# Kernel optimization log

Measured on AMD Instinct MI355X. Metric: run time of the kernel, lower is better.

Reference implementation:

```python
import jax, jax.numpy as jnp
import numpy as np

N = 50000      # nodes
E = 800000     # edges (avg degree 16)
D_IN, D_H, D_OUT = 128, 96, 32


def _lin(x, W, b):
    return x @ W.T + b


def _transformer_conv(x, src, dst, Wq, bq, Wk, bk, Wv, bv, Ws, bs, n):
    # PyG TransformerConv, heads=1: q_i . k_j / sqrt(d), segment softmax over
    # incoming edges of each target node, weighted sum of values, plus skip.
    q = _lin(x, Wq, bq)            # [N, d]
    k = _lin(x, Wk, bk)            # [N, d]
    v = _lin(x, Wv, bv)            # [N, d]
    d = q.shape[-1]
    score = jnp.sum(q[dst] * k[src], axis=-1) / jnp.sqrt(jnp.float32(d))  # [E]
    m = jax.ops.segment_max(score, dst, num_segments=n)                   # [N]
    m = jnp.where(jnp.isneginf(m), 0.0, m)   # isolated nodes
    e = jnp.exp(score - m[dst])                                           # [E]
    denom = jax.ops.segment_sum(e, dst, num_segments=n)                   # [N]
    alpha = e / jnp.maximum(denom[dst], 1e-16)                            # [E]
    agg = jax.ops.segment_sum(alpha[:, None] * v[src], dst, num_segments=n)
    return agg + _lin(x, Ws, bs)   # root weight (skip connection)


def setup_inputs() -> dict:
    key = jax.random.key(0)
    ks = jax.random.split(key, 32)
    x = jax.random.normal(ks[0], (N, D_IN), dtype=jnp.float32)
    edge_index = jax.random.randint(ks[1], (2, E), 0, N, dtype=jnp.int64)
    dims = [(D_IN, D_H), (D_H, D_H), (D_H, D_OUT)]
    inp = {"x": x, "edge_index": edge_index}
    ki = 2
    for li, (fi, fo) in enumerate(dims, start=1):
        s = 1.0 / np.sqrt(fi)
        for nm in ("Wq", "Wk", "Wv", "Ws"):
            inp[f"{nm}{li}"] = jax.random.normal(ks[ki], (fo, fi), dtype=jnp.float32) * s
            ki += 1
        for nm in ("bq", "bk", "bv", "bs"):
            inp[f"{nm}{li}"] = jnp.zeros((fo,), dtype=jnp.float32)
    return inp


def reference(x, edge_index,
              Wq1, Wk1, Wv1, Ws1, bq1, bk1, bv1, bs1,
              Wq2, Wk2, Wv2, Ws2, bq2, bk2, bv2, bs2,
              Wq3, Wk3, Wv3, Ws3, bq3, bk3, bv3, bs3):
    src, dst = edge_index[0], edge_index[1]
    h = jax.nn.relu(_transformer_conv(x, src, dst, Wq1, bq1, Wk1, bk1, Wv1, bv1, Ws1, bs1, N))
    h = jax.nn.relu(_transformer_conv(h, src, dst, Wq2, bq2, Wk2, bk2, Wv2, bv2, Ws2, bs2, N))
    h = _transformer_conv(h, src, dst, Wq3, bq3, Wk3, bk3, Wv3, bv3, Ws3, bs3, N)
    return jax.nn.log_softmax(h, axis=1)
```

## Files before the change

### kernel.cpp

```cpp
#include <hip/hip_runtime.h>
#include <math.h>

typedef __attribute__((ext_vector_type(8))) __bf16 bf16x8;
typedef __attribute__((ext_vector_type(8))) short short8;
typedef __attribute__((ext_vector_type(4))) float f32x4;
typedef unsigned int uint;
typedef unsigned short ushort;
typedef unsigned char uchar;


__device__ inline bf16x8 ld_bf8(const ushort* p){
  short8 s = *reinterpret_cast<const short8*>(p);
  return __builtin_bit_cast(bf16x8, s);
}

__device__ inline ushort f2bf(float f){
  return __builtin_bit_cast(ushort, (__bf16)f);
}
__device__ inline uint pack2bf(float a, float b){
  return (uint)f2bf(a) | ((uint)f2bf(b) << 16);
}
__device__ inline float bf_lo(uint u){ return __builtin_bit_cast(float, u << 16); }
__device__ inline float bf_hi(uint u){ return __builtin_bit_cast(float, u & 0xFFFF0000u); }

template<int S>
__device__ inline float unp8(uint w){
  return __builtin_amdgcn_cvt_f32_fp8((int)w, S);
}
__device__ inline uint pk8(float a, float b, float c, float d){
  int r = 0;
  r = __builtin_amdgcn_cvt_pk_fp8_f32(a, b, r, false);
  r = __builtin_amdgcn_cvt_pk_fp8_f32(c, d, r, true);
  return (uint)r;
}


__global__ __launch_bounds__(256) void k_bucketA(const int* __restrict__ dst,
                                                 int* __restrict__ gbh, int E){
  __shared__ int cnt[256];
  cnt[threadIdx.x] = 0;
  __syncthreads();
  for (int e = blockIdx.x * blockDim.x + threadIdx.x; e < E; e += gridDim.x * blockDim.x)
    atomicAdd(&cnt[dst[e] >> 8], 1);
  __syncthreads();
  int c = cnt[threadIdx.x];
  if (c > 0) atomicAdd(&gbh[threadIdx.x], c);
}

__global__ __launch_bounds__(256) void k_bscan(const int* __restrict__ gbh,
                                               int* __restrict__ gbase,
                                               int* __restrict__ gcur, int NB, int E){
  __shared__ int wsum[4];
  int t = threadIdx.x;
  int c = (t < NB) ? gbh[t] : 0;
  int lane = t & 63, wv = t >> 6;
  int incl = c;
  #pragma unroll
  for (int o = 1; o < 64; o <<= 1){
    int x = __shfl_up(incl, o);
    if (lane >= o) incl += x;
  }
  if (lane == 63) wsum[wv] = incl;
  __syncthreads();
  int woff = 0;
  for (int w = 0; w < wv; ++w) woff += wsum[w];
  int excl = woff + incl - c;
  if (t < NB){ gbase[t] = excl; gcur[t] = excl; }
  if (t == 0) gbase[NB] = E;
}

#define CS_CHUNK 4096
__global__ __launch_bounds__(256) void k_bucketB(const int* __restrict__ src,
                                                 const int* __restrict__ dst,
                                                 int* __restrict__ gcur,
                                                 uint* __restrict__ epack, int E){
  __shared__ int cnt[256];
  __shared__ int wcur[256];
  const int b0 = blockIdx.x * CS_CHUNK;
  const int b1 = (b0 + CS_CHUNK < E) ? b0 + CS_CHUNK : E;
  cnt[threadIdx.x] = 0;
  __syncthreads();
  for (int e = b0 + threadIdx.x; e < b1; e += 256)
    atomicAdd(&cnt[dst[e] >> 8], 1);
  __syncthreads();
  int c = cnt[threadIdx.x];
  int base = (c > 0) ? atomicAdd(&gcur[threadIdx.x], c) : 0;
  wcur[threadIdx.x] = base;
  __syncthreads();
  for (int e = b0 + threadIdx.x; e < b1; e += 256){
    int d = dst[e];
    int s = src[e];
    int pos = atomicAdd(&wcur[d >> 8], 1);
    epack[pos] = ((uint)d << 16) | (uint)(s & 0xFFFF);
  }
}

__global__ __launch_bounds__(256) void k_bucketC(const uint* __restrict__ epack,
                                                 const int* __restrict__ gbase,
                                                 int* __restrict__ offs,
                                                 ushort* __restrict__ srclist,
                                                 int N, int E){
  __shared__ int cnt[256];
  __shared__ int wcur[256];
  __shared__ int wsum[4];
  const int b = blockIdx.x;
  const int lo = gbase[b], hi = gbase[b + 1];
  cnt[threadIdx.x] = 0;
  __syncthreads();
  for (int i = lo + threadIdx.x; i < hi; i += 256)
    atomicAdd(&cnt[(epack[i] >> 16) & 255], 1);
  __syncthreads();
  int c = cnt[threadIdx.x];
  int lane = threadIdx.x & 63, wv = threadIdx.x >> 6;
  int incl = c;
  #pragma unroll
  for (int o = 1; o < 64; o <<= 1){
    int x = __shfl_up(incl, o);
    if (lane >= o) incl += x;
  }
  if (lane == 63) wsum[wv] = incl;
  __syncthreads();
  int woff = 0;
  for (int w = 0; w < wv; ++w) woff += wsum[w];
  int excl = lo + woff + incl - c;
  int d = (b << 8) + threadIdx.x;
  if (d < N) offs[d] = excl;
  wcur[threadIdx.x] = excl;
  __syncthreads();
  for (int i = lo + threadIdx.x; i < hi; i += 256){
    uint ep = epack[i];
    int pos = atomicAdd(&wcur[(ep >> 16) & 255], 1);
    srclist[pos] = (ushort)(ep & 0xFFFF);
  }
  if (b == 0 && threadIdx.x == 0) offs[N] = E;
}


struct WSet { const float* src[12]; ushort* dst[12]; int n[12]; };

__global__ __launch_bounds__(256) void k_castw(WSet ws){
  int m = blockIdx.y;
  int n = ws.n[m];
  const float* s = ws.src[m];
  ushort* d = ws.dst[m];
  for (int i = blockIdx.x * blockDim.x + threadIdx.x; i < n; i += gridDim.x * blockDim.x)
    d[i] = f2bf(s[i]);
}


template<int KT, int NT, bool F32IN>
__global__ __launch_bounds__(256) void k_projmfma(
    const ushort* __restrict__ hin, const float* __restrict__ hinf, int N,
    const ushort* __restrict__ Wq, const ushort* __restrict__ Wk,
    const ushort* __restrict__ Wv, const ushort* __restrict__ Wsk,
    const float* __restrict__ bq, const float* __restrict__ bk,
    const float* __restrict__ bv, const float* __restrict__ bs,
    ushort* __restrict__ qo, uchar* __restrict__ kv8,
    ushort* __restrict__ so, int kvstB)
{
  constexpr int K  = KT * 32;
  constexpr int FO = NT * 16;
  const int wv   = threadIdx.x >> 6;
  const int lane = threadIdx.x & 63;
  const int r16  = lane & 15;
  const int kg   = lane >> 4;

  const ushort* W = (wv == 0) ? Wq : (wv == 1) ? Wk : (wv == 2) ? Wv : Wsk;
  const float*  b = (wv == 0) ? bq : (wv == 1) ? bk : (wv == 2) ? bv : bs;

  bf16x8 bf[NT][KT];
  #pragma unroll
  for (int nt = 0; nt < NT; ++nt)
    #pragma unroll
    for (int kt = 0; kt < KT; ++kt)
      bf[nt][kt] = ld_bf8(W + (size_t)(nt * 16 + r16) * K + kt * 32 + kg * 8);

  float4 bias[NT];
  #pragma unroll
  for (int nt = 0; nt < NT; ++nt)
    bias[nt] = *reinterpret_cast<const float4*>(b + nt * 16 + kg * 4);

  const int MT = N >> 4;
  for (int mt = blockIdx.x; mt < MT; mt += gridDim.x){
    const int row0 = mt * 16;
    bf16x8 af[KT];
    #pragma unroll
    for (int kt = 0; kt < KT; ++kt){
      if constexpr (F32IN){
        const float* xr = hinf + (size_t)(row0 + r16) * K + kt * 32 + kg * 8;
        float4 a = reinterpret_cast<const float4*>(xr)[0];
        float4 c = reinterpret_cast<const float4*>(xr)[1];
        uint4 u;
        u.x = pack2bf(a.x, a.y); u.y = pack2bf(a.z, a.w);
        u.z = pack2bf(c.x, c.y); u.w = pack2bf(c.z, c.w);
        af[kt] = __builtin_bit_cast(bf16x8, u);
      } else {
        af[kt] = ld_bf8(hin + (size_t)(row0 + r16) * K + kt * 32 + kg * 8);
      }
    }

    f32x4 acc[NT];
    #pragma unroll
    for (int nt = 0; nt < NT; ++nt){
      acc[nt][0] = bias[nt].x; acc[nt][1] = bias[nt].y;
      acc[nt][2] = bias[nt].z; acc[nt][3] = bias[nt].w;
    }
    #pragma unroll
    for (int nt = 0; nt < NT; ++nt)
      #pragma unroll
      for (int kt = 0; kt < KT; ++kt)
        acc[nt] = __builtin_amdgcn_mfma_f32_16x16x32_bf16(bf[nt][kt], af[kt], acc[nt], 0, 0, 0);

    const int row = row0 + r16;
    if (wv == 0 || wv == 3){
      ushort* out = (wv == 0) ? qo : so;
      #pragma unroll
      for (int nt = 0; nt < NT; ++nt){
        uint* p = reinterpret_cast<uint*>(out + (size_t)row * FO + nt * 16 + kg * 4);
        p[0] = pack2bf(acc[nt][0], acc[nt][1]);
        p[1] = pack2bf(acc[nt][2], acc[nt][3]);
      }
    } else {
      const int voff = (wv == 2) ? FO : 0;
      #pragma unroll
      for (int nt = 0; nt < NT; ++nt){
        uint u = pk8(acc[nt][0], acc[nt][1], acc[nt][2], acc[nt][3]);
        *reinterpret_cast<uint*>(kv8 + (size_t)row * kvstB + voff + nt * 16 + kg * 4) = u;
      }
    }
  }
}


template<int FO, int MODE>
__global__ __launch_bounds__(256) void k_attn3(
    const ushort* __restrict__ qb, const uchar* __restrict__ kv,
    const ushort* __restrict__ skipb, const int* __restrict__ offs,
    const ushort* __restrict__ srclist, void* __restrict__ outp,
    int N, float scale)
{
  constexpr int G   = 8;
  constexpr int FPL = FO / G;
  constexpr int KW  = FPL / 4;
  constexpr int KVB = 2 * FO;
  const int lane = threadIdx.x & 63;
  const int sub  = lane & 7;
  const int node = (blockIdx.x * (blockDim.x >> 6) + (threadIdx.x >> 6)) * 8 + (lane >> 3);
  const bool nv  = node < N;
  const int nodec = nv ? node : 0;

  const uint2* qrow = reinterpret_cast<const uint2*>(qb + (size_t)nodec * FO + sub * FPL);
  float qf[FPL];
  #pragma unroll
  for (int w = 0; w < KW; ++w){
    uint2 t = qrow[w];
    qf[4 * w]     = bf_lo(t.x); qf[4 * w + 1] = bf_hi(t.x);
    qf[4 * w + 2] = bf_lo(t.y); qf[4 * w + 3] = bf_hi(t.y);
  }

  float m = -INFINITY, l = 0.f;
  float acc[FPL];
  #pragma unroll
  for (int f = 0; f < FPL; ++f) acc[f] = 0.f;

  const int e0 = nv ? offs[node] : 0;
  const int e1 = nv ? offs[node + 1] : 0;

  uint kA[4][KW], vA[4][KW], kB[4][KW], vB[4][KW];

  auto DOLOAD = [&](int eb, uint (*Kr)[KW], uint (*Vr)[KW]){
    #pragma unroll
    for (int i = 0; i < 4; ++i){
      int ee = eb + i;
      int ec = (ee < e1) ? ee : (e1 - 1);
      int j = srclist[ec];
      const uchar* row = kv + (size_t)j * KVB;
      const uint* rk = reinterpret_cast<const uint*>(row + sub * FPL);
      const uint* rv = reinterpret_cast<const uint*>(row + FO + sub * FPL);
      #pragma unroll
      for (int w = 0; w < KW; ++w){
        Kr[i][w] = rk[w];
        Vr[i][w] = rv[w];
      }
    }
  };

  auto COMPUTE = [&](uint (*Kr)[KW], uint (*Vr)[KW], int ebase){
    float s[4];
    #pragma unroll
    for (int i = 0; i < 4; ++i){
      float t = 0.f;
      #pragma unroll
      for (int w = 0; w < KW; ++w){
        uint kwd = Kr[i][w];
        t = fmaf(qf[4 * w],     unp8<0>(kwd), t);
        t = fmaf(qf[4 * w + 1], unp8<1>(kwd), t);
        t = fmaf(qf[4 * w + 2], unp8<2>(kwd), t);
        t = fmaf(qf[4 * w + 3], unp8<3>(kwd), t);
      }
      s[i] = t;
    }
    #pragma unroll
    for (int o = 1; o < G; o <<= 1){
      s[0] += __shfl_xor(s[0], o);
      s[1] += __shfl_xor(s[1], o);
      s[2] += __shfl_xor(s[2], o);
      s[3] += __shfl_xor(s[3], o);
    }
    s[0] = s[0] * scale;
    s[1] = (ebase + 1 < e1) ? s[1] * scale : -1e30f;
    s[2] = (ebase + 2 < e1) ? s[2] * scale : -1e30f;
    s[3] = (ebase + 3 < e1) ? s[3] * scale : -1e30f;

    float mnew = fmaxf(fmaxf(m, s[0]), fmaxf(fmaxf(s[1], s[2]), s[3]));
    float sfac = __expf(m - mnew);
    float p4[4];
    p4[0] = __expf(s[0] - mnew);
    p4[1] = __expf(s[1] - mnew);
    p4[2] = __expf(s[2] - mnew);
    p4[3] = __expf(s[3] - mnew);
    l = l * sfac + (p4[0] + p4[1]) + (p4[2] + p4[3]);
    #pragma unroll
    for (int f = 0; f < FPL; ++f) acc[f] *= sfac;
    #pragma unroll
    for (int i = 0; i < 4; ++i){
      #pragma unroll
      for (int w = 0; w < KW; ++w){
        uint vwd = Vr[i][w];
        acc[4 * w]     = fmaf(p4[i], unp8<0>(vwd), acc[4 * w]);
        acc[4 * w + 1] = fmaf(p4[i], unp8<1>(vwd), acc[4 * w + 1]);
        acc[4 * w + 2] = fmaf(p4[i], unp8<2>(vwd), acc[4 * w + 2]);
        acc[4 * w + 3] = fmaf(p4[i], unp8<3>(vwd), acc[4 * w + 3]);
      }
    }
    m = mnew;
  };

  if (e0 < e1){
    int e = e0;
    DOLOAD(e, kA, vA);
    for (;;){
      int en = e + 4;
      bool more = en < e1;
      if (more) DOLOAD(en, kB, vB);
      COMPUTE(kA, vA, e);
      e = en;
      if (!more) break;
      en = e + 4;
      more = en < e1;
      if (more) DOLOAD(en, kA, vA);
      COMPUTE(kB, vB, e);
      e = en;
      if (!more) break;
    }
  }

  float inv = 1.f / fmaxf(l, 1e-16f);
  const uint2* srow = reinterpret_cast<const uint2*>(skipb + (size_t)nodec * FO + sub * FPL);
  float val[FPL];
  #pragma unroll
  for (int w = 0; w < KW; ++w){
    uint2 t = srow[w];
    val[4 * w]     = bf_lo(t.x) + acc[4 * w] * inv;
    val[4 * w + 1] = bf_hi(t.x) + acc[4 * w + 1] * inv;
    val[4 * w + 2] = bf_lo(t.y) + acc[4 * w + 2] * inv;
    val[4 * w + 3] = bf_hi(t.y) + acc[4 * w + 3] * inv;
  }

  if (MODE == 0){
    if (nv){
      uint2* orow = reinterpret_cast<uint2*>((ushort*)outp + (size_t)node * FO + sub * FPL);
      #pragma unroll
      for (int w = 0; w < KW; ++w){
        uint2 o;
        o.x = pack2bf(fmaxf(val[4 * w], 0.f),     fmaxf(val[4 * w + 1], 0.f));
        o.y = pack2bf(fmaxf(val[4 * w + 2], 0.f), fmaxf(val[4 * w + 3], 0.f));
        orow[w] = o;
      }
    }
  } else {
    float mx = -INFINITY;
    #pragma unroll
    for (int f = 0; f < FPL; ++f) mx = fmaxf(mx, val[f]);
    #pragma unroll
    for (int o = 1; o < G; o <<= 1) mx = fmaxf(mx, __shfl_xor(mx, o));
    float ssum = 0.f;
    #pragma unroll
    for (int f = 0; f < FPL; ++f) ssum += __expf(val[f] - mx);
    #pragma unroll
    for (int o = 1; o < G; o <<= 1) ssum += __shfl_xor(ssum, o);
    float lg = __logf(ssum);
    if (nv){
      float* orow = (float*)outp + (size_t)node * FO + sub * FPL;
      #pragma unroll
      for (int f = 0; f < FPL; ++f) orow[f] = val[f] - mx - lg;
    }
  }
}


extern "C" void kernel_launch(void* const* d_in, const int* in_sizes, int n_in,
                              void* d_out, int out_size, void* d_ws, size_t ws_size,
                              hipStream_t stream)
{
  const float* x  = (const float*)d_in[0];
  const int*   ei = (const int*)d_in[1];
  const int N = in_sizes[0] / 128;
  const int E = in_sizes[1] / 2;

  const float* W1[4]; const float* b1[4];
  const float* W2[4]; const float* b2[4];
  const float* W3[4]; const float* b3[4];
  for (int i = 0; i < 4; ++i){
    W1[i] = (const float*)d_in[2 + i];   b1[i] = (const float*)d_in[6 + i];
    W2[i] = (const float*)d_in[10 + i];  b2[i] = (const float*)d_in[14 + i];
    W3[i] = (const float*)d_in[18 + i];  b3[i] = (const float*)d_in[22 + i];
  }

  size_t off = 0;
  auto alloc = [&](size_t bytes) -> void* {
    void* p = (char*)d_ws + off;
    off = (off + bytes + 255) & ~(size_t)255;
    return p;
  };
  const int NB = (N + 255) / 256;
  int* offs       = (int*)alloc(((size_t)N + 1) * 4);
  int* gbh        = (int*)alloc(256 * 4);
  int* gbase      = (int*)alloc(260 * 4);
  int* gcur       = (int*)alloc(256 * 4);
  uint* epack     = (uint*)alloc((size_t)E * 4);
  ushort* srclist = (ushort*)alloc((size_t)E * 2);
  ushort* qb  = (ushort*)alloc((size_t)N * 96 * 2);
  uchar*  kvb = (uchar*)alloc((size_t)N * 192);
  ushort* sb  = (ushort*)alloc((size_t)N * 96 * 2);
  ushort* hb  = (ushort*)alloc((size_t)N * 128 * 2);
  ushort* wb  = (ushort*)alloc((size_t)98304 * 2);

  ushort* Wb1[4]; ushort* Wb2[4]; ushort* Wb3[4];
  for (int i = 0; i < 4; ++i){
    Wb1[i] = wb + (size_t)i * 12288;
    Wb2[i] = wb + 49152 + (size_t)i * 9216;
    Wb3[i] = wb + 49152 + 36864 + (size_t)i * 3072;
  }

  WSet wset;
  for (int i = 0; i < 4; ++i){
    wset.src[i]     = W1[i]; wset.dst[i]     = Wb1[i]; wset.n[i]     = 12288;
    wset.src[4 + i] = W2[i]; wset.dst[4 + i] = Wb2[i]; wset.n[4 + i] = 9216;
    wset.src[8 + i] = W3[i]; wset.dst[8 + i] = Wb3[i]; wset.n[8 + i] = 3072;
  }
  k_castw<<<dim3(48, 12), dim3(256), 0, stream>>>(wset);

  const int* esrc = ei;
  const int* edst = ei + E;
  hipMemsetAsync(gbh, 0, 256 * 4, stream);
  k_bucketA<<<dim3(392), dim3(256), 0, stream>>>(edst, gbh, E);
  k_bscan<<<dim3(1), dim3(256), 0, stream>>>(gbh, gbase, gcur, NB, E);
  const int nCB = (E + CS_CHUNK - 1) / CS_CHUNK;
  k_bucketB<<<dim3(nCB), dim3(256), 0, stream>>>(esrc, edst, gcur, epack, E);
  k_bucketC<<<dim3(NB), dim3(256), 0, stream>>>(epack, gbase, offs, srclist, N, E);

  float* outf = (float*)d_out;
  const float sc96 = 1.0f / sqrtf(96.f);
  const float sc32 = 1.0f / sqrtf(32.f);

  const int MT = N / 16;
  const int tpb = (MT + 1023) / 1024;
  const int gridP = (MT + tpb - 1) / tpb;
  const int gridA = (N + 31) / 32;

  k_projmfma<4, 6, true><<<dim3(gridP), dim3(256), 0, stream>>>(nullptr, x, N,
      Wb1[0], Wb1[1], Wb1[2], Wb1[3], b1[0], b1[1], b1[2], b1[3],
      qb, kvb, sb, 192);
  k_attn3<96, 0><<<dim3(gridA), dim3(256), 0, stream>>>(qb, kvb, sb, offs, srclist, hb, N, sc96);

  k_projmfma<3, 6, false><<<dim3(gridP), dim3(256), 0, stream>>>(hb, nullptr, N,
      Wb2[0], Wb2[1], Wb2[2], Wb2[3], b2[0], b2[1], b2[2], b2[3],
      qb, kvb, sb, 192);
  k_attn3<96, 0><<<dim3(gridA), dim3(256), 0, stream>>>(qb, kvb, sb, offs, srclist, hb, N, sc96);

  k_projmfma<3, 2, false><<<dim3(gridP), dim3(256), 0, stream>>>(hb, nullptr, N,
      Wb3[0], Wb3[1], Wb3[2], Wb3[3], b3[0], b3[1], b3[2], b3[3],
      qb, kvb, sb, 64);
  k_attn3<32, 1><<<dim3(gridA), dim3(256), 0, stream>>>(qb, kvb, sb, offs, srclist, outf, N, sc32);
}
```

Measured before the change: 199.5 us.

## Stage projection weights in LDS and split matrices across grid y

The projection kernel now assigns one weight matrix per block (blockIdx.y) and stages that matrix in padded shared memory. Each of the four waves processes its own 16-row tile, instead of four waves sharing a tile with one matrix each. B fragments are read from LDS per MFMA rather than held in registers, which lowers register pressure but adds LDS traffic and a per-block weight load. The grid is fixed at 384x4 blocks. The memset of the bucket histogram is also replaced by a tiny zeroing kernel.

```diff
diff --git a/kernel.cpp b/kernel.cpp
--- a/kernel.cpp
+++ b/kernel.cpp
@@ -34,6 +34,10 @@
   return (uint)r;
 }
 
+
+__global__ void k_zero(int* __restrict__ p, int n){
+  if ((int)threadIdx.x < n) p[threadIdx.x] = 0;
+}
 
 __global__ __launch_bounds__(256) void k_bucketA(const int* __restrict__ dst,
                                                  int* __restrict__ gbh, int E){
@@ -159,29 +163,34 @@
     ushort* __restrict__ so, int kvstB)
 {
   constexpr int K  = KT * 32;
+  constexpr int PS = K + 8;
   constexpr int FO = NT * 16;
+  __shared__ ushort wlds[FO * PS];
+
+  const int mat = blockIdx.y;
+  const ushort* W = (mat == 0) ? Wq : (mat == 1) ? Wk : (mat == 2) ? Wv : Wsk;
+  const float*  b = (mat == 0) ? bq : (mat == 1) ? bk : (mat == 2) ? bv : bs;
+
+  for (int idx = threadIdx.x; idx < FO * (K / 8); idx += 256){
+    int row = idx / (K / 8);
+    int c8  = idx - row * (K / 8);
+    *reinterpret_cast<short8*>(&wlds[row * PS + c8 * 8]) =
+        *reinterpret_cast<const short8*>(W + (size_t)row * K + c8 * 8);
+  }
+  __syncthreads();
+
   const int wv   = threadIdx.x >> 6;
   const int lane = threadIdx.x & 63;
   const int r16  = lane & 15;
   const int kg   = lane >> 4;
 
-  const ushort* W = (wv == 0) ? Wq : (wv == 1) ? Wk : (wv == 2) ? Wv : Wsk;
-  const float*  b = (wv == 0) ? bq : (wv == 1) ? bk : (wv == 2) ? bv : bs;
-
-  bf16x8 bf[NT][KT];
-  #pragma unroll
-  for (int nt = 0; nt < NT; ++nt)
-    #pragma unroll
-    for (int kt = 0; kt < KT; ++kt)
-      bf[nt][kt] = ld_bf8(W + (size_t)(nt * 16 + r16) * K + kt * 32 + kg * 8);
-
   float4 bias[NT];
   #pragma unroll
   for (int nt = 0; nt < NT; ++nt)
     bias[nt] = *reinterpret_cast<const float4*>(b + nt * 16 + kg * 4);
 
   const int MT = N >> 4;
-  for (int mt = blockIdx.x; mt < MT; mt += gridDim.x){
+  for (int mt = blockIdx.x * 4 + wv; mt < MT; mt += gridDim.x * 4){
     const int row0 = mt * 16;
     bf16x8 af[KT];
     #pragma unroll
@@ -208,12 +217,14 @@
     #pragma unroll
     for (int nt = 0; nt < NT; ++nt)
       #pragma unroll
-      for (int kt = 0; kt < KT; ++kt)
-        acc[nt] = __builtin_amdgcn_mfma_f32_16x16x32_bf16(bf[nt][kt], af[kt], acc[nt], 0, 0, 0);
+      for (int kt = 0; kt < KT; ++kt){
+        bf16x8 bfr = ld_bf8(&wlds[(nt * 16 + r16) * PS + kt * 32 + kg * 8]);
+        acc[nt] = __builtin_amdgcn_mfma_f32_16x16x32_bf16(bfr, af[kt], acc[nt], 0, 0, 0);
+      }
 
     const int row = row0 + r16;
-    if (wv == 0 || wv == 3){
-      ushort* out = (wv == 0) ? qo : so;
+    if (mat == 0 || mat == 3){
+      ushort* out = (mat == 0) ? qo : so;
       #pragma unroll
       for (int nt = 0; nt < NT; ++nt){
         uint* p = reinterpret_cast<uint*>(out + (size_t)row * FO + nt * 16 + kg * 4);
@@ -221,7 +232,7 @@
         p[1] = pack2bf(acc[nt][2], acc[nt][3]);
       }
     } else {
-      const int voff = (wv == 2) ? FO : 0;
+      const int voff = (mat == 2) ? FO : 0;
       #pragma unroll
       for (int nt = 0; nt < NT; ++nt){
         uint u = pk8(acc[nt][0], acc[nt][1], acc[nt][2], acc[nt][3]);
@@ -453,7 +464,7 @@
 
   const int* esrc = ei;
   const int* edst = ei + E;
-  hipMemsetAsync(gbh, 0, 256 * 4, stream);
+  k_zero<<<dim3(1), dim3(256), 0, stream>>>(gbh, 256);
   k_bucketA<<<dim3(392), dim3(256), 0, stream>>>(edst, gbh, E);
   k_bscan<<<dim3(1), dim3(256), 0, stream>>>(gbh, gbase, gcur, NB, E);
   const int nCB = (E + CS_CHUNK - 1) / CS_CHUNK;
@@ -464,22 +475,19 @@
   const float sc96 = 1.0f / sqrtf(96.f);
   const float sc32 = 1.0f / sqrtf(32.f);
 
-  const int MT = N / 16;
-  const int tpb = (MT + 1023) / 1024;
-  const int gridP = (MT + tpb - 1) / tpb;
   const int gridA = (N + 31) / 32;
 
-  k_projmfma<4, 6, true><<<dim3(gridP), dim3(256), 0, stream>>>(nullptr, x, N,
+  k_projmfma<4, 6, true><<<dim3(384, 4), dim3(256), 0, stream>>>(nullptr, x, N,
       Wb1[0], Wb1[1], Wb1[2], Wb1[3], b1[0], b1[1], b1[2], b1[3],
       qb, kvb, sb, 192);
   k_attn3<96, 0><<<dim3(gridA), dim3(256), 0, stream>>>(qb, kvb, sb, offs, srclist, hb, N, sc96);
 
-  k_projmfma<3, 6, false><<<dim3(gridP), dim3(256), 0, stream>>>(hb, nullptr, N,
+  k_projmfma<3, 6, false><<<dim3(384, 4), dim3(256), 0, stream>>>(hb, nullptr, N,
       Wb2[0], Wb2[1], Wb2[2], Wb2[3], b2[0], b2[1], b2[2], b2[3],
       qb, kvb, sb, 192);
   k_attn3<96, 0><<<dim3(gridA), dim3(256), 0, stream>>>(qb, kvb, sb, offs, srclist, hb, N, sc96);
 
-  k_projmfma<3, 2, false><<<dim3(gridP), dim3(256), 0, stream>>>(hb, nullptr, N,
+  k_projmfma<3, 2, false><<<dim3(384, 4), dim3(256), 0, stream>>>(hb, nullptr, N,
       Wb3[0], Wb3[1], Wb3[2], Wb3[3], b3[0], b3[1], b3[2], b3[3],
       qb, kvb, sb, 64);
   k_attn3<32, 1><<<dim3(gridA), dim3(256), 0, stream>>>(qb, kvb, sb, offs, srclist, outf, N, sc32);
```

Result: faster. 186.0 us (-6.7%).
